# Kernel optimization log

Measured on AMD Instinct MI355X. Metric: run time of the kernel, lower is better.

## Reference

```python
import jax, jax.numpy as jnp
import numpy as np

B, L, D, K_F = 2, 1024, 768, 16  # batch, seq_len, n_embd, num_eigh**2
N_FFT = 2048


def setup_inputs() -> dict:
    key = jax.random.key(0)
    k1, k2, k3, k4 = jax.random.split(key, 4)
    x = jax.random.normal(k1, (B, L, D), dtype=jnp.float32)
    phi = jax.random.normal(k2, (L, K_F), dtype=jnp.float32) * 0.1
    M_phi_plus = jax.random.normal(k3, (K_F, D, D), dtype=jnp.float32) * (1.0 / np.sqrt(K_F * D))
    M_phi_minus = jax.random.normal(k4, (K_F, D, D), dtype=jnp.float32) * (1.0 / np.sqrt(K_F * D))
    return {"x": x, "phi": phi, "M_phi_plus": M_phi_plus, "M_phi_minus": M_phi_minus, "n": N_FFT}


def _convolve(u, v, n):
    """FFT causal convolution with K spectral filters (flash-stu `convolve`, use_approx=False).
    u: [B, L, D] inputs; v: [L, K] filters; n: FFT length (>= 2L-1 padded pow2).
    Returns U_plus, U_minus: [B, L, K, D].
    """
    b, l, d = u.shape
    sgn = jnp.where(jnp.arange(l) % 2 == 0, 1.0, -1.0).astype(u.dtype)  # alternating +/-
    # Stack the plain and sign-modulated signals: [B, L, 1, D, 2]
    U = jnp.stack([u, u * sgn[None, :, None]], axis=-1)[:, :, None, :, :]
    Uf = jnp.fft.rfft(U, n=n, axis=1)                      # [B, F, 1, D, 2] complex
    vf = jnp.fft.rfft(v, n=n, axis=0)[None, :, :, None, None]  # [1, F, K, 1, 1]
    conv = jnp.fft.irfft(vf * Uf, n=n, axis=1)[:, :l]      # [B, L, K, D, 2]
    U_plus = conv[..., 0]
    U_minus = conv[..., 1] * sgn[None, :, None, None]
    return U_plus, U_minus


def reference(x, phi, M_phi_plus, M_phi_minus, n):
    U_plus, U_minus = _convolve(x, phi, n)
    # tensordot(U, M, dims=([2,3],[0,2])): contract eigenmode k and input channel i
    spectral_plus = jnp.einsum('blki,koi->blo', U_plus, M_phi_plus)
    spectral_minus = jnp.einsum('blki,koi->blo', U_minus, M_phi_minus)
    return spectral_plus + spectral_minus
```

## Files before the change

kernel.cpp:

```cpp
#include <hip/hip_runtime.h>
#include <hip/hip_fp16.h>

typedef unsigned short u16;
typedef unsigned int   u32;
typedef _Float16 f16;
typedef __attribute__((ext_vector_type(8))) f16 f16x8;
typedef __attribute__((ext_vector_type(2))) __fp16 fp16x2;
typedef __attribute__((ext_vector_type(4))) float f32x4;

#define B_SZ  2
#define L_SEQ 1024
#define D_EMB 768
#define KF    16
#define MDIM  (B_SZ * L_SEQ)
#define KROW  (KF * D_EMB)
#define MELEM ((size_t)KF * D_EMB * D_EMB)
#define NTILE 96
#define PT_SZ 16384

__device__ __forceinline__ void gload16(const void* g, void* l) {
    __builtin_amdgcn_global_load_lds(
        (const __attribute__((address_space(1))) u32*)g,
        (__attribute__((address_space(3))) u32*)l, 16, 0, 0);
}

__global__ __launch_bounds__(256) void stu_setup(const float* __restrict__ x,
                                                 const float* __restrict__ phi,
                                                 u16* __restrict__ xT,
                                                 u16* __restrict__ Ttab) {
    __shared__ __align__(16) float xs[64][68];
    const int bid = blockIdx.x;
    const int tid = threadIdx.x;

    if (bid < 384) {
        const int s0 = (bid & 15) << 6;
        const int d0 = ((bid >> 4) % 12) << 6;
        const int b  = bid / 192;

#pragma unroll
        for (int j = 0; j < 4; ++j) {
            int c = tid + (j << 8);
            int row = c >> 4;
            int col = (c & 15) << 2;
            *(float4*)&xs[row][col] =
                *(const float4*)&x[((size_t)b * L_SEQ + s0 + row) * D_EMB + d0 + col];
        }
        __syncthreads();

        const int dl = tid >> 2;
        const int ss = (tid & 3) << 4;
        const int dg = d0 + dl;
        const int xorv = (dg & 7) << 3;

        union { u16 v[16]; uint4 q[2]; } pk;
#pragma unroll
        for (int u = 0; u < 16; ++u)
            pk.v[u] = __half_as_ushort(__float2half(xs[ss + u][dl]));

        size_t base = (size_t)b * D_EMB * L_SEQ + (size_t)dg * L_SEQ + s0;
        *(uint4*)&xT[base + ( ss      ^ xorv)] = pk.q[0];
        *(uint4*)&xT[base + ((ss + 8) ^ xorv)] = pk.q[1];
    } else {
        const int f = bid - 384;
        const int q = f & 15;
        const int k = f >> 4;
        const int tt  = tid >> 2;
        const int ss0 = (tid & 3) << 4;

        union { u16 v[16]; uint4 q4[2]; } pk;
#pragma unroll
        for (int u = 0; u < 16; ++u) {
            int s = (q << 6) + tt - (ss0 + u);
            float v = (s >= 0 && s < L_SEQ) ? phi[s * KF + k] : 0.f;
            pk.v[u] = __half_as_ushort(__float2half(v));
        }
        const int xorv = (tt & 7) << 3;
        u16* tile = Ttab + (((size_t)k * 16 + q) << 12);
        *(uint4*)&tile[(tt << 6) + ( ss0      ^ xorv)] = pk.q4[0];
        *(uint4*)&tile[(tt << 6) + ((ss0 + 8) ^ xorv)] = pk.q4[1];
    }
}

__global__ __launch_bounds__(256) void stu_conv_mcvt(
        const u16* __restrict__ xT, const u16* __restrict__ Ttab,
        u16* __restrict__ Up, u16* __restrict__ Um,
        const float* __restrict__ Mp, const float* __restrict__ Mm,
        u16* __restrict__ Hp, u16* __restrict__ Hm) {
    __shared__ __align__(16) u16 Xs[2][192 * 64];
    __shared__ __align__(16) u16 Tps[2][64 * 64];

    const int bid = blockIdx.x;
    const int tid = threadIdx.x;

    if (bid < 512) {
        const size_t n8 = MELEM / 8;
        size_t i = (size_t)bid * 256 + tid;
        const size_t stride = (size_t)512 * 256;
        for (size_t cc = i; cc < n8; cc += stride) {
            const size_t g = cc << 3;
            {
                const float4 a0 = *(const float4*)&Mp[g];
                const float4 a1 = *(const float4*)&Mp[g + 4];
                union { fp16x2 h2[4]; uint4 q; } u;
                u.h2[0] = __builtin_amdgcn_cvt_pkrtz(a0.x, a0.y);
                u.h2[1] = __builtin_amdgcn_cvt_pkrtz(a0.z, a0.w);
                u.h2[2] = __builtin_amdgcn_cvt_pkrtz(a1.x, a1.y);
                u.h2[3] = __builtin_amdgcn_cvt_pkrtz(a1.z, a1.w);
                *(uint4*)&Hp[g] = u.q;
            }
            {
                const float4 a0 = *(const float4*)&Mm[g];
                const float4 a1 = *(const float4*)&Mm[g + 4];
                union { fp16x2 h2[4]; uint4 q; } u;
                u.h2[0] = __builtin_amdgcn_cvt_pkrtz(a0.x, a0.y);
                u.h2[1] = __builtin_amdgcn_cvt_pkrtz(a0.z, a0.w);
                u.h2[2] = __builtin_amdgcn_cvt_pkrtz(a1.x, a1.y);
                u.h2[3] = __builtin_amdgcn_cvt_pkrtz(a1.z, a1.w);
                *(uint4*)&Hm[g] = u.q;
            }
        }
        return;
    }

    const int c    = bid - 512;
    const int xcd  = c & 7;
    const int w    = c >> 3;
    const int ti   = 15 - (w >> 4);
    const int t0   = ti << 6;
    const int inner = w & 15;
    const int bk   = (xcd << 2) + (inner >> 2);
    const int b    = bk >> 4;
    const int k    = bk & 15;
    const int d0   = (inner & 3) * 192;

    const int lane = tid & 63;
    const int wid  = tid >> 6;
    const int wr   = wid >> 1;
    const int wc   = wid & 1;
    const int lr   = lane & 15;
    const int lk   = lane >> 4;

    const u32 xm = (lr & 1) ? 0x00008000u : 0x80000000u;

    f32x4 acc[2][2][6];
#pragma unroll
    for (int s = 0; s < 2; ++s)
#pragma unroll
        for (int m = 0; m < 2; ++m)
#pragma unroll
            for (int n = 0; n < 6; ++n)
                acc[s][m][n] = (f32x4){0.f, 0.f, 0.f, 0.f};

    const u16* xTb = xT + (size_t)b * D_EMB * L_SEQ + (size_t)d0 * L_SEQ;
    const u16* Tpk = Ttab + ((size_t)k << 16);

    auto stageX = [&](int buf, int r0) {
#pragma unroll
        for (int j = 0; j < 6; ++j) {
            int cc = tid + (j << 8);
            gload16(xTb + (size_t)(cc >> 3) * L_SEQ + r0 + ((cc & 7) << 3),
                    &Xs[buf][cc << 3]);
        }
    };
    auto stageT = [&](int buf, int q) {
        const u16* tp = Tpk + ((size_t)q << 12);
        gload16(tp + (tid << 3),         &Tps[buf][tid << 3]);
        gload16(tp + ((tid + 256) << 3), &Tps[buf][(tid + 256) << 3]);
    };

    stageX(0, 0);
    stageT(0, ti);
    __syncthreads();

    int cur = 0;
    for (int r0 = 0; r0 <= t0; r0 += 64) {
        if (r0 < t0) {
            stageT(cur ^ 1, ((t0 - r0) >> 6) - 1);
            stageX(cur ^ 1, r0 + 64);
        }

        const char* XsC = (const char*)&Xs[cur][0];
        const char* TpC = (const char*)&Tps[cur][0];

#pragma unroll
        for (int kk = 0; kk < 2; ++kk) {
            f16x8 bfr[6];
#pragma unroll
            for (int n = 0; n < 6; ++n) {
                const int row = wc * 96 + (n << 4) + lr;
                const int boff = ((kk << 6) + (lk << 4)) ^ ((row & 7) << 4);
                bfr[n] = *(const f16x8*)(XsC + row * 128 + boff);
            }
#pragma unroll
            for (int m = 0; m < 2; ++m) {
                const int rowt = (wr << 5) + (m << 4) + lr;
                const int aoff = ((kk << 6) + (lk << 4)) ^ ((rowt & 7) << 4);
                const f16x8 ap = *(const f16x8*)(TpC + rowt * 128 + aoff);
                union { f16x8 h; u32 wv[4]; } cv;
                cv.h = ap;
#pragma unroll
                for (int qd = 0; qd < 4; ++qd) cv.wv[qd] ^= xm;
                const f16x8 am = cv.h;
#pragma unroll
                for (int n = 0; n < 6; ++n) {
                    acc[0][m][n] = __builtin_amdgcn_mfma_f32_16x16x32_f16(
                        ap, bfr[n], acc[0][m][n], 0, 0, 0);
                    acc[1][m][n] = __builtin_amdgcn_mfma_f32_16x16x32_f16(
                        am, bfr[n], acc[1][m][n], 0, 0, 0);
                }
            }
        }
        __syncthreads();
        cur ^= 1;
    }

#pragma unroll
    for (int m = 0; m < 2; ++m) {
        const int trow = t0 + (wr << 5) + (m << 4) + (lk << 2);
#pragma unroll
        for (int n = 0; n < 6; ++n) {
            const int col = d0 + wc * 96 + (n << 4) + lr;
#pragma unroll
            for (int j = 0; j < 4; ++j) {
                size_t idx = ((size_t)(b * L_SEQ + trow + j) * KF + k) * D_EMB + col;
                Up[idx] = __half_as_ushort(__float2half(acc[0][m][n][j]));
                Um[idx] = __half_as_ushort(__float2half(acc[1][m][n][j]));
            }
        }
    }
}

__global__ __launch_bounds__(256) void stu_spectral_mfma(
        const u16* __restrict__ Up, const u16* __restrict__ Um,
        const u16* __restrict__ Mhp, const u16* __restrict__ Mhm,
        float* __restrict__ out, u16* __restrict__ P, int usePartial) {
    __shared__ __align__(16) u16 As[128 * 64];
    __shared__ __align__(16) u16 Bs[128 * 64];

    const int h   = blockIdx.x;
    const int z   = h & 7;
    const int rem = h >> 3;
    const int o0  = (rem % 6) << 7;
    const int m0  = (rem / 6) << 7;
    const int sign = z & 1;
    const int k0 = (z >> 1) << 2;

    const u16* A    = sign ? Um : Up;
    const u16* Bsrc = sign ? Mhm : Mhp;

    const int tid  = threadIdx.x;
    const int lane = tid & 63;
    const int wid  = tid >> 6;
    const int wr   = wid >> 1;
    const int wc   = wid & 1;
    const int lr   = lane & 15;
    const int lk   = lane >> 4;

    f32x4 acc[4][4];
#pragma unroll
    for (int m = 0; m < 4; ++m)
#pragma unroll
        for (int n = 0; n < 4; ++n)
            acc[m][n] = (f32x4){0.f, 0.f, 0.f, 0.f};

    for (int k = k0; k < k0 + 4; ++k) {
        const u16* Ak = A + (size_t)m0 * KROW + k * D_EMB;
        const u16* Bk = Bsrc + (size_t)k * D_EMB * D_EMB + (size_t)o0 * D_EMB;

        for (int ic = 0; ic < D_EMB; ic += 64) {
            __syncthreads();
#pragma unroll
            for (int j = 0; j < 4; ++j) {
                const int c = tid + (j << 8);
                const int row = c >> 3;
                const int off = ((c & 7) ^ (row & 7)) << 3;
                gload16(Ak + (size_t)row * KROW + ic + off, &As[c << 3]);
                gload16(Bk + (size_t)row * D_EMB + ic + off, &Bs[c << 3]);
            }
            __syncthreads();

#pragma unroll
            for (int kk = 0; kk < 2; ++kk) {
                f16x8 af[4], bf[4];
#pragma unroll
                for (int m = 0; m < 4; ++m) {
                    const int row = wr * 64 + (m << 4) + lr;
                    const int boff = (((kk << 2) + lk) ^ (row & 7)) << 4;
                    af[m] = *(const f16x8*)((const char*)&As[0] + row * 128 + boff);
                }
#pragma unroll
                for (int n = 0; n < 4; ++n) {
                    const int row = wc * 64 + (n << 4) + lr;
                    const int boff = (((kk << 2) + lk) ^ (row & 7)) << 4;
                    bf[n] = *(const f16x8*)((const char*)&Bs[0] + row * 128 + boff);
                }
#pragma unroll
                for (int m = 0; m < 4; ++m)
#pragma unroll
                    for (int n = 0; n < 4; ++n)
                        acc[m][n] = __builtin_amdgcn_mfma_f32_16x16x32_f16(
                            af[m], bf[n], acc[m][n], 0, 0, 0);
            }
        }
    }

    if (usePartial) {
        u16* Pt = P + (size_t)h * PT_SZ;
#pragma unroll
        for (int m = 0; m < 4; ++m) {
            const int rowl = wr * 64 + (m << 4) + (lk << 2);
#pragma unroll
            for (int n = 0; n < 4; ++n) {
                const int coll = wc * 64 + (n << 4) + lr;
#pragma unroll
                for (int j = 0; j < 4; ++j)
                    Pt[(rowl + j) * 128 + coll] =
                        __half_as_ushort(__float2half(acc[m][n][j]));
            }
        }
    } else {
#pragma unroll
        for (int m = 0; m < 4; ++m) {
            const int row = m0 + wr * 64 + (m << 4) + (lk << 2);
#pragma unroll
            for (int n = 0; n < 4; ++n) {
                const int col = o0 + wc * 64 + (n << 4) + lr;
#pragma unroll
                for (int j = 0; j < 4; ++j)
                    atomicAdd(&out[(size_t)(row + j) * D_EMB + col], acc[m][n][j]);
            }
        }
    }
}

__global__ __launch_bounds__(256) void stu_reduce(const u16* __restrict__ P,
                                                  float* __restrict__ out) {
    const size_t total = (size_t)MDIM * D_EMB;
    size_t idx = (size_t)blockIdx.x * 256 + threadIdx.x;
    const size_t stride = (size_t)gridDim.x * 256;
    for (; idx < total; idx += stride) {
        const int row = (int)(idx / D_EMB);
        const int col = (int)(idx % D_EMB);
        const int tile = (row >> 7) * 6 + (col >> 7);
        const u16* p = P + (size_t)tile * 8 * PT_SZ + ((row & 127) << 7) + (col & 127);
        float s = 0.f;
#pragma unroll
        for (int z = 0; z < 8; ++z)
            s += __half2float(__ushort_as_half(p[z * PT_SZ]));
        out[idx] = s;
    }
}

extern "C" void kernel_launch(void* const* d_in, const int* in_sizes, int n_in,
                              void* d_out, int out_size, void* d_ws, size_t ws_size,
                              hipStream_t stream) {
    const float* x   = (const float*)d_in[0];
    const float* phi = (const float*)d_in[1];
    const float* Mp  = (const float*)d_in[2];
    const float* Mm  = (const float*)d_in[3];
    float* out = (float*)d_out;

    const size_t S = (size_t)MDIM * KROW;
    u16* Up   = (u16*)d_ws;
    u16* Um   = Up + S;
    u16* Mhp  = Um + S;
    u16* Mhm  = Mhp + MELEM;
    u16* xT   = Mhm + MELEM;
    u16* Ttab = xT + (size_t)B_SZ * D_EMB * L_SEQ;
    u16* Part = Ttab + (size_t)KF * 16 * 4096;

    const size_t elems_needed = 2 * S + 2 * MELEM + 1572864 + 1048576 + 12582912;
    const int usePartial = (ws_size >= elems_needed * sizeof(u16)) ? 1 : 0;

    if (!usePartial)
        (void)hipMemsetAsync(d_out, 0, (size_t)out_size * sizeof(float), stream);

    stu_setup<<<dim3(640), dim3(256), 0, stream>>>(x, phi, xT, Ttab);

    stu_conv_mcvt<<<dim3(2560), dim3(256), 0, stream>>>(
        xT, Ttab, Up, Um, Mp, Mm, Mhp, Mhm);

    stu_spectral_mfma<<<dim3(NTILE * 8), dim3(256), 0, stream>>>(
        Up, Um, Mhp, Mhm, out, Part, usePartial);

    if (usePartial)
        stu_reduce<<<dim3(1536), dim3(256), 0, stream>>>(Part, out);
}
```

Measured before the change: 169.0 us.

## Enlarge causal-conv Toeplitz tile to 128 output rows with 512-thread blocks

The causal convolution GEMM now computes 128 output time rows per block instead of 64, using 512 threads (8 waves), so each staged X tile is reused across twice as many Toeplitz rows. The Toeplitz filter table is rebuilt as 128x64 tiles, which doubles its workspace footprint. The M-conversion blocks are halved in count but doubled in width. This halves redundant X loads and block count at the cost of more LDS per block and coarser causal load balance.

```diff
diff --git a/kernel.cpp b/kernel.cpp
--- a/kernel.cpp
+++ b/kernel.cpp
@@ -17,6 +17,7 @@
 #define MELEM ((size_t)KF * D_EMB * D_EMB)
 #define NTILE 96
 #define PT_SZ 16384
+#define TT_K  (16 * 8192)
 
 __device__ __forceinline__ void gload16(const void* g, void* l) {
     __builtin_amdgcn_global_load_lds(
@@ -61,41 +62,42 @@
         *(uint4*)&xT[base + ( ss      ^ xorv)] = pk.q[0];
         *(uint4*)&xT[base + ((ss + 8) ^ xorv)] = pk.q[1];
     } else {
-        const int f = bid - 384;
-        const int q = f & 15;
-        const int k = f >> 4;
-        const int tt  = tid >> 2;
-        const int ss0 = (tid & 3) << 4;
-
-        union { u16 v[16]; uint4 q4[2]; } pk;
-#pragma unroll
-        for (int u = 0; u < 16; ++u) {
-            int s = (q << 6) + tt - (ss0 + u);
+        const int f  = bid - 384;
+        const int qi = f & 15;
+        const int k  = f >> 4;
+        const int tt  = tid >> 1;
+        const int ss0 = (tid & 1) << 5;
+
+        union { u16 v[32]; uint4 q4[4]; } pk;
+#pragma unroll
+        for (int u = 0; u < 32; ++u) {
+            int s = ((qi - 1) << 6) + tt - (ss0 + u);
             float v = (s >= 0 && s < L_SEQ) ? phi[s * KF + k] : 0.f;
             pk.v[u] = __half_as_ushort(__float2half(v));
         }
         const int xorv = (tt & 7) << 3;
-        u16* tile = Ttab + (((size_t)k * 16 + q) << 12);
-        *(uint4*)&tile[(tt << 6) + ( ss0      ^ xorv)] = pk.q4[0];
-        *(uint4*)&tile[(tt << 6) + ((ss0 + 8) ^ xorv)] = pk.q4[1];
-    }
-}
-
-__global__ __launch_bounds__(256) void stu_conv_mcvt(
+        u16* tile = Ttab + ((size_t)k * TT_K) + ((size_t)qi << 13);
+#pragma unroll
+        for (int u = 0; u < 4; ++u)
+            *(uint4*)&tile[(tt << 6) + ((ss0 + (u << 3)) ^ xorv)] = pk.q4[u];
+    }
+}
+
+__global__ __launch_bounds__(512) void stu_conv_mcvt(
         const u16* __restrict__ xT, const u16* __restrict__ Ttab,
         u16* __restrict__ Up, u16* __restrict__ Um,
         const float* __restrict__ Mp, const float* __restrict__ Mm,
         u16* __restrict__ Hp, u16* __restrict__ Hm) {
     __shared__ __align__(16) u16 Xs[2][192 * 64];
-    __shared__ __align__(16) u16 Tps[2][64 * 64];
+    __shared__ __align__(16) u16 Tps[2][128 * 64];
 
     const int bid = blockIdx.x;
     const int tid = threadIdx.x;
 
-    if (bid < 512) {
+    if (bid < 256) {
         const size_t n8 = MELEM / 8;
-        size_t i = (size_t)bid * 256 + tid;
-        const size_t stride = (size_t)512 * 256;
+        size_t i = (size_t)bid * 512 + tid;
+        const size_t stride = (size_t)256 * 512;
         for (size_t cc = i; cc < n8; cc += stride) {
             const size_t g = cc << 3;
             {
@@ -122,11 +124,11 @@
         return;
     }
 
-    const int c    = bid - 512;
+    const int c    = bid - 256;
     const int xcd  = c & 7;
     const int w    = c >> 3;
-    const int ti   = 15 - (w >> 4);
-    const int t0   = ti << 6;
+    const int ti   = 7 - (w >> 4);
+    const int t0   = ti << 7;
     const int inner = w & 15;
     const int bk   = (xcd << 2) + (inner >> 2);
     const int b    = bk >> 4;
@@ -152,31 +154,33 @@
                 acc[s][m][n] = (f32x4){0.f, 0.f, 0.f, 0.f};
 
     const u16* xTb = xT + (size_t)b * D_EMB * L_SEQ + (size_t)d0 * L_SEQ;
-    const u16* Tpk = Ttab + ((size_t)k << 16);
+    const u16* Tpk = Ttab + (size_t)k * TT_K;
 
     auto stageX = [&](int buf, int r0) {
 #pragma unroll
-        for (int j = 0; j < 6; ++j) {
-            int cc = tid + (j << 8);
+        for (int j = 0; j < 3; ++j) {
+            int cc = tid + (j << 9);
             gload16(xTb + (size_t)(cc >> 3) * L_SEQ + r0 + ((cc & 7) << 3),
                     &Xs[buf][cc << 3]);
         }
     };
-    auto stageT = [&](int buf, int q) {
-        const u16* tp = Tpk + ((size_t)q << 12);
+    auto stageT = [&](int buf, int qi) {
+        const u16* tp = Tpk + ((size_t)qi << 13);
         gload16(tp + (tid << 3),         &Tps[buf][tid << 3]);
-        gload16(tp + ((tid + 256) << 3), &Tps[buf][(tid + 256) << 3]);
+        gload16(tp + ((tid + 512) << 3), &Tps[buf][(tid + 512) << 3]);
     };
 
     stageX(0, 0);
-    stageT(0, ti);
+    stageT(0, 2 * ti + 1);
     __syncthreads();
 
+    const int jmax = 2 * ti + 1;
     int cur = 0;
-    for (int r0 = 0; r0 <= t0; r0 += 64) {
-        if (r0 < t0) {
-            stageT(cur ^ 1, ((t0 - r0) >> 6) - 1);
-            stageX(cur ^ 1, r0 + 64);
+    int qi  = 2 * ti + 1;
+    for (int j = 0; j <= jmax; ++j) {
+        if (j < jmax) {
+            stageT(cur ^ 1, qi - 1);
+            stageX(cur ^ 1, (j + 1) << 6);
         }
 
         const char* XsC = (const char*)&Xs[cur][0];
@@ -212,6 +216,7 @@
         }
         __syncthreads();
         cur ^= 1;
+        --qi;
     }
 
 #pragma unroll
@@ -367,9 +372,9 @@
     u16* Mhm  = Mhp + MELEM;
     u16* xT   = Mhm + MELEM;
     u16* Ttab = xT + (size_t)B_SZ * D_EMB * L_SEQ;
-    u16* Part = Ttab + (size_t)KF * 16 * 4096;
-
-    const size_t elems_needed = 2 * S + 2 * MELEM + 1572864 + 1048576 + 12582912;
+    u16* Part = Ttab + (size_t)KF * TT_K;
+
+    const size_t elems_needed = 2 * S + 2 * MELEM + 1572864 + 2097152 + 12582912;
     const int usePartial = (ws_size >= elems_needed * sizeof(u16)) ? 1 : 0;
 
     if (!usePartial)
@@ -377,7 +382,7 @@
 
     stu_setup<<<dim3(640), dim3(256), 0, stream>>>(x, phi, xT, Ttab);
 
-    stu_conv_mcvt<<<dim3(2560), dim3(256), 0, stream>>>(
+    stu_conv_mcvt<<<dim3(1280), dim3(512), 0, stream>>>(
         xT, Ttab, Up, Um, Mp, Mm, Mhp, Mhm);
 
     stu_spectral_mfma<<<dim3(NTILE * 8), dim3(256), 0, stream>>>(
```

After: 177.3 us. 1.05x slower.
